# Optimization experiments

Hardware: AMD Instinct MI355X
Metric: run time of the kernel (lower is better)

Reference implementation:

```python
import jax, jax.numpy as jnp
import numpy as np

T, B, H = 512, 128, 512

def setup_inputs() -> dict:
    key = jax.random.key(0)
    k1, k2, k3, k4 = jax.random.split(key, 4)
    s = 1.0 / np.sqrt(H)
    x = jax.random.normal(k1, (T, B, H), dtype=jnp.float32)
    resets = jax.random.randint(k2, (T, B), 0, 2).astype(bool)
    Wi = jax.random.normal(k3, (H, 3 * H), dtype=jnp.float32) * s
    bi = jnp.zeros((3 * H,), dtype=jnp.float32)
    Wh = jax.random.normal(k4, (H, 3 * H), dtype=jnp.float32) * s
    bhn = jnp.zeros((H,), dtype=jnp.float32)
    h0 = jnp.zeros((B, H), dtype=jnp.float32)
    return {"x": x, "resets": resets, "Wi": Wi, "bi": bi, "Wh": Wh, "bhn": bhn, "h0": h0}

def reference(x, resets, Wi, bi, Wh, bhn, h0):
    # Scanned flax GRUCell with per-step carry reset (reset -> zeros carry).
    def step(h, inp):
        xt, rt = inp                                   # xt: [B,H], rt: [B]
        h = jnp.where(rt[:, None], jnp.zeros_like(h), h)
        gi = xt @ Wi + bi                              # [B,3H]
        gh = h @ Wh                                    # [B,3H]
        ir, iz, inn = jnp.split(gi, 3, axis=-1)
        hr, hz, hn = jnp.split(gh, 3, axis=-1)
        r = jax.nn.sigmoid(ir + hr)
        z = jax.nn.sigmoid(iz + hz)
        n = jnp.tanh(inn + r * (hn + bhn))             # bias only on h 'n' gate (flax GRUCell)
        new_h = (1.0 - z) * n + z * h
        return new_h, new_h
    _, ys = jax.lax.scan(step, h0, (x, resets))
    return ys                                          # [T,B,H]
```

## Files before the change

### kernel.cpp

```cpp
#include <hip/hip_runtime.h>


typedef _Float16 f16;
typedef _Float16 f16x8 __attribute__((ext_vector_type(8)));
typedef float f32x4 __attribute__((ext_vector_type(4)));
typedef float f32x16 __attribute__((ext_vector_type(16)));

#define TT 512
#define BB 128
#define HH 512
#define H3 1536
#define TBR 65536
#define NC 64
#define CL 8
#define NR 8192
static const size_t PL = (size_t)TBR * HH;

__device__ __forceinline__ float sigf(float x) { return 1.f / (1.f + __expf(-x)); }

__global__ __launch_bounds__(256) void k_prep(
    const float* __restrict__ Wi, const float* __restrict__ Wh,
    const int* __restrict__ resets,
    f16* __restrict__ WiT, f16* __restrict__ WhT,
    int* __restrict__ fr, int* __restrict__ cnt) {
  int idx = blockIdx.x * 256 + threadIdx.x;
  if (idx < HH * H3) {
    int n = idx >> 9;
    int k = idx & (HH - 1);
    WiT[idx] = (f16)Wi[(size_t)k * H3 + n];
    WhT[idx] = (f16)Wh[(size_t)k * H3 + n];
  }
  if (idx < NR) {
    int c = idx >> 7, b = idx & 127;
    int f = CL;
    for (int s = CL - 1; s >= 0; --s)
      if (resets[(c * CL + s) * BB + b]) f = s;
    fr[idx] = f;
    atomicAdd(&cnt[f], 1);
  }
}

__global__ __launch_bounds__(256) void k_prepB(
    const f16* __restrict__ WhT, f16* __restrict__ WhTf) {
  int u = blockIdx.x * 256 + threadIdx.x;
  int l = u & 63;
  int kb = (u >> 6) & 31;
  int t = u >> 11;
  f16x8 v = *(const f16x8*)(WhT + (size_t)(t * 32 + (l & 31)) * HH +
                            kb * 16 + (l >> 5) * 8);
  *(f16x8*)(WhTf + (size_t)u * 8) = v;
}

__global__ void k_sort(int* __restrict__ cnt) {
  int st = 0;
  cnt[16 + 8] = 0;
  for (int f = 7; f >= 0; --f) {
    st += cnt[f + 1];
    cnt[16 + f] = st;
  }
  for (int f = 1; f <= 8; ++f) cnt[32 + f] = cnt[16 + f];
}

__global__ __launch_bounds__(256) void k_scatter(
    const int* __restrict__ fr, int* __restrict__ cnt, int* __restrict__ list,
    int* __restrict__ slist) {
  int idx = blockIdx.x * 256 + threadIdx.x;
  if (idx < NR) {
    int f = fr[idx];
    if (f >= 1) {
      int pos = atomicAdd(&cnt[32 + f], 1);
      list[pos] = idx;
    }
    int c = idx >> 7;
    if (f == CL && c < NC - 1 && (c == 0 || fr[idx - BB] < CL)) {
      int p = atomicAdd(&cnt[48], 1);
      slist[p] = idx;
    }
  }
}

__global__ __launch_bounds__(256) void k_gemm_gi(
    const float* __restrict__ x, const f16* __restrict__ WiT,
    const float* __restrict__ bi, f16* __restrict__ gi) {
  __shared__ __align__(16) f16 xs[64 * 512];
  const int tid = threadIdx.x;
  const int lane = tid & 63;
  const int w = tid >> 6;
  const size_t i0 = (size_t)blockIdx.x * 64;

  {
    const int row = tid >> 2;
    const int mi = row >> 5;
    const int lin = (row & 31) + ((tid & 1) << 5);
    const int koct = (tid & 3) * 8;
#pragma unroll 4
    for (int kb32 = 0; kb32 < 16; ++kb32) {
      const int k = kb32 * 32 + koct;
      const float* xp = x + (i0 + row) * HH + k;
      float4 v0 = *(const float4*)xp;
      float4 v1 = *(const float4*)(xp + 4);
      f16x8 a8;
      a8[0] = (f16)v0.x; a8[1] = (f16)v0.y; a8[2] = (f16)v0.z; a8[3] = (f16)v0.w;
      a8[4] = (f16)v1.x; a8[5] = (f16)v1.y; a8[6] = (f16)v1.z; a8[7] = (f16)v1.w;
      *(f16x8*)&xs[((k >> 4) * 2 + mi) * 512 + lin * 8] = a8;
    }
  }
  __syncthreads();

  const int ln31 = lane & 31;
  const int kh8 = (lane >> 5) * 8;
  const int r4 = (lane >> 5) * 4;

  for (int jt = 0; jt < 6; ++jt) {
    const int j0 = jt * 256 + w * 64;
    f32x16 acc[2][2] = {};
    const f16* bp0 = WiT + (size_t)(j0 + ln31) * HH + kh8;
    const f16* bp1 = bp0 + (size_t)32 * HH;
#pragma unroll 4
    for (int kb = 0; kb < 32; ++kb) {
      f16x8 af0 = *(const f16x8*)&xs[(kb * 2 + 0) * 512 + lane * 8];
      f16x8 af1 = *(const f16x8*)&xs[(kb * 2 + 1) * 512 + lane * 8];
      f16x8 bf0 = *(const f16x8*)(bp0 + kb * 16);
      f16x8 bf1 = *(const f16x8*)(bp1 + kb * 16);
      acc[0][0] = __builtin_amdgcn_mfma_f32_32x32x16_f16(af0, bf0, acc[0][0], 0, 0, 0);
      acc[0][1] = __builtin_amdgcn_mfma_f32_32x32x16_f16(af0, bf1, acc[0][1], 0, 0, 0);
      acc[1][0] = __builtin_amdgcn_mfma_f32_32x32x16_f16(af1, bf0, acc[1][0], 0, 0, 0);
      acc[1][1] = __builtin_amdgcn_mfma_f32_32x32x16_f16(af1, bf1, acc[1][1], 0, 0, 0);
    }
#pragma unroll
    for (int ni = 0; ni < 2; ++ni) {
      const int j = j0 + ni * 32 + ln31;
      const float bj = bi[j];
      const int p = j >> 9, jj = j & 511;
#pragma unroll
      for (int mi = 0; mi < 2; ++mi)
#pragma unroll
        for (int r = 0; r < 16; ++r) {
          const int row = mi * 32 + (r & 3) + 8 * (r >> 2) + r4;
          gi[(size_t)p * PL + (i0 + row) * HH + jj] =
              (f16)(acc[mi][ni][r] + bj);
        }
    }
  }
}

__global__ __launch_bounds__(256) void k_step0(
    const int* __restrict__ resets, const f16* __restrict__ gi,
    const float* __restrict__ bhn, float* __restrict__ out,
    f16* __restrict__ hA) {
  int gid = blockIdx.x * 256 + threadIdx.x;
  int row = gid >> 6;
  int c8 = (gid & 63) * 8;
  int c = row >> 7, b = row & 127;
  size_t girow = (size_t)c * 1024 + b;
  const f16x8 g0 = *(const f16x8*)(gi + girow * HH + c8);
  const f16x8 g1 = *(const f16x8*)(gi + PL + girow * HH + c8);
  const f16x8 g2 = *(const f16x8*)(gi + 2 * PL + girow * HH + c8);
  const int z1 = resets[(c * CL + 1) * BB + b];
  float4 o[2];
  f16x8 hn;
#pragma unroll
  for (int u = 0; u < 8; ++u) {
    float r = sigf((float)g0[u]);
    float z = sigf((float)g1[u]);
    float n = tanhf((float)g2[u] + r * bhn[c8 + u]);
    float h = (1.f - z) * n;
    ((float*)o)[u] = h;
    hn[u] = z1 ? (f16)0.f : (f16)h;
  }
  *(float4*)(out + girow * HH + c8) = o[0];
  *(float4*)(out + girow * HH + c8 + 4) = o[1];
  *(f16x8*)(hA + (size_t)row * HH + c8) = hn;
}

__global__ __launch_bounds__(256, 2) void k_phase1(
    int s, const int* __restrict__ resets, const f16* __restrict__ WhT,
    const f16* __restrict__ gi, const float* __restrict__ bhn,
    float* __restrict__ out, const f16* __restrict__ hrd,
    f16* __restrict__ hwr) {
  __shared__ __align__(16) f16 As[128 * 40];
  __shared__ __align__(16) f16 Bs[192 * 40];
  const int tid = threadIdx.x;
  const int lane = tid & 63;
  const int w = tid >> 6;
  const int c = blockIdx.x;
  const int j0 = blockIdx.y * 64;
  const int t = c * CL + s;
  const int wm = (w & 1) * 64;
  const int wn = (w >> 1) * 32;
  const int fr = lane & 15;
  const int q8 = (lane >> 4) * 8;

  f32x4 acc[3][4][2] = {};

  for (int kb = 0; kb < 16; ++kb) {
    const int k0 = kb * 32;
#pragma unroll
    for (int uu = 0; uu < 2; ++uu) {
      int u = tid + uu * 256;
      int row = u >> 2, oc = (u & 3) * 8;
      *(f16x8*)&As[row * 40 + oc] =
          *(const f16x8*)(hrd + ((size_t)(c * BB + row)) * HH + k0 + oc);
    }
#pragma unroll
    for (int uu = 0; uu < 3; ++uu) {
      int u = tid + uu * 256;
      int row = u >> 2, oc = (u & 3) * 8;
      int g = row >> 6, j = j0 + (row & 63);
      *(f16x8*)&Bs[row * 40 + oc] =
          *(const f16x8*)(WhT + ((size_t)(g * HH + j)) * HH + k0 + oc);
    }
    __syncthreads();
    f16x8 af[4];
#pragma unroll
    for (int mi = 0; mi < 4; ++mi)
      af[mi] = *(const f16x8*)&As[(wm + mi * 16 + fr) * 40 + q8];
    f16x8 bf[3][2];
#pragma unroll
    for (int g = 0; g < 3; ++g)
#pragma unroll
      for (int ni = 0; ni < 2; ++ni)
        bf[g][ni] = *(const f16x8*)&Bs[(g * 64 + wn + ni * 16 + fr) * 40 + q8];
#pragma unroll
    for (int g = 0; g < 3; ++g)
#pragma unroll
      for (int mi = 0; mi < 4; ++mi)
#pragma unroll
        for (int ni = 0; ni < 2; ++ni)
          acc[g][mi][ni] = __builtin_amdgcn_mfma_f32_16x16x32_f16(
              af[mi], bf[g][ni], acc[g][mi][ni], 0, 0, 0);
    __syncthreads();
  }

  const int trow = (lane >> 4) * 4;
#pragma unroll
  for (int mi = 0; mi < 4; ++mi)
#pragma unroll
    for (int ni = 0; ni < 2; ++ni) {
      const int j = j0 + wn + ni * 16 + fr;
      const float bh = bhn[j];
#pragma unroll
      for (int r = 0; r < 4; ++r) {
        const int b = wm + mi * 16 + trow + r;
        const size_t girow = (size_t)c * 1024 + (size_t)s * BB + b;
        const float gr = (float)gi[girow * HH + j];
        const float gz = (float)gi[PL + girow * HH + j];
        const float gn = (float)gi[2 * PL + girow * HH + j];
        const float hp = (float)hrd[((size_t)(c * BB + b)) * HH + j];
        const float rr = sigf(gr + acc[0][mi][ni][r]);
        const float zz = sigf(gz + acc[1][mi][ni][r]);
        const float nn = tanhf(gn + rr * (acc[2][mi][ni][r] + bh));
        const float hnew = (1.f - zz) * nn + zz * hp;
        out[girow * HH + j] = hnew;
        int zr = (s < 7) ? resets[(t + 1) * BB + b] : 0;
        hwr[((size_t)(c * BB + b)) * HH + j] = zr ? (f16)0.f : (f16)hnew;
      }
    }
}

__global__ __launch_bounds__(256) void k_bound(
    const int* __restrict__ fr, const f16* __restrict__ hend,
    const float* __restrict__ h0, f16* __restrict__ hin) {
  int gid = blockIdx.x * 256 + threadIdx.x;
  int row = gid >> 6;
  int o8 = (gid & 63) * 8;
  int c = row >> 7, b = row & 127;
  if (c == 0) {
    const float* hp = h0 + (size_t)b * HH + o8;
    float4 v0 = *(const float4*)hp;
    float4 v1 = *(const float4*)(hp + 4);
    f16x8 h;
    h[0] = (f16)v0.x; h[1] = (f16)v0.y; h[2] = (f16)v0.z; h[3] = (f16)v0.w;
    h[4] = (f16)v1.x; h[5] = (f16)v1.y; h[6] = (f16)v1.z; h[7] = (f16)v1.w;
    *(f16x8*)(hin + (size_t)row * HH + o8) = h;
  } else if (fr[row - BB] < CL) {
    *(f16x8*)(hin + (size_t)row * HH + o8) =
        *(const f16x8*)(hend + (size_t)(row - BB) * HH + o8);
  }
}

__global__ __launch_bounds__(1024) void k_chain2(
    const int* __restrict__ fr, const f16* __restrict__ hend,
    const f16* __restrict__ WhTf, const f16* __restrict__ gi,
    const float* __restrict__ bhn, const float* __restrict__ h0,
    f16* __restrict__ hin, const int* __restrict__ slist,
    const int* __restrict__ cnt) {
  const int count = cnt[48];
  const int nbat = (count + 31) >> 5;
  __shared__ __align__(16) f16 hsA[32 * 512];
  __shared__ int ch[32];
  __shared__ int anyact;
  const int tid = threadIdx.x;
  const int lane = tid & 63;
  const int w = tid >> 6;
  const int nc = lane & 31;
  const int hi = lane >> 5;

  for (int bat = blockIdx.x; bat < nbat; bat += gridDim.x) {
    if (tid < 32) {
      int r = bat * 32 + tid;
      ch[tid] = (r < count) ? slist[r] : -1;
    }
    __syncthreads();
    for (int u = tid; u < 32 * 64; u += 1024) {
      int m = u >> 6, o8 = (u & 63) * 8;
      int cr = ch[m];
      f16x8 h = {};
      if (cr >= 0) {
        if ((cr >> 7) == 0) {
          const float* hp = h0 + (size_t)(cr & 127) * HH + o8;
          float4 v0 = *(const float4*)hp;
          float4 v1 = *(const float4*)(hp + 4);
          h[0] = (f16)v0.x; h[1] = (f16)v0.y; h[2] = (f16)v0.z; h[3] = (f16)v0.w;
          h[4] = (f16)v1.x; h[5] = (f16)v1.y; h[6] = (f16)v1.z; h[7] = (f16)v1.w;
        } else {
          h = *(const f16x8*)(hend + (size_t)(cr - BB) * HH + o8);
        }
      }
      *(f16x8*)&hsA[(o8 >> 4) * 512 + (m + ((o8 >> 3) & 1) * 32) * 8] = h;
    }
    __syncthreads();

    while (true) {
      for (int s = 0; s < CL; ++s) {
        f32x16 a0 = {}, a1 = {}, a2 = {};
        const f16* b0p = WhTf + ((size_t)(w)*32 * 64 + lane) * 8;
        const f16* b1p = WhTf + ((size_t)(16 + w) * 32 * 64 + lane) * 8;
        const f16* b2p = WhTf + ((size_t)(32 + w) * 32 * 64 + lane) * 8;
#pragma unroll 4
        for (int kb = 0; kb < 32; ++kb) {
          f16x8 af = *(const f16x8*)&hsA[kb * 512 + lane * 8];
          f16x8 bf0 = *(const f16x8*)(b0p + (size_t)kb * 512);
          f16x8 bf1 = *(const f16x8*)(b1p + (size_t)kb * 512);
          f16x8 bf2 = *(const f16x8*)(b2p + (size_t)kb * 512);
          a0 = __builtin_amdgcn_mfma_f32_32x32x16_f16(af, bf0, a0, 0, 0, 0);
          a1 = __builtin_amdgcn_mfma_f32_32x32x16_f16(af, bf1, a1, 0, 0, 0);
          a2 = __builtin_amdgcn_mfma_f32_32x32x16_f16(af, bf2, a2, 0, 0, 0);
        }
        __syncthreads();
        const int j = w * 32 + nc;
        const float bh = bhn[j];
#pragma unroll
        for (int r = 0; r < 16; ++r) {
          const int m = (r & 3) + 8 * (r >> 2) + 4 * hi;
          const int cr = ch[m];
          const size_t girow =
              (cr >= 0)
                  ? ((size_t)(cr >> 7) * 1024 + (size_t)s * BB + (cr & 127))
                  : 0;
          const float gr = (float)gi[girow * HH + j];
          const float gz = (float)gi[PL + girow * HH + j];
          const float gn = (float)gi[2 * PL + girow * HH + j];
          const int ha =
              (j >> 4) * 512 + (m + ((j >> 3) & 1) * 32) * 8 + (j & 7);
          const float hp = (float)hsA[ha];
          const float rr = sigf(gr + a0[r]);
          const float zz = sigf(gz + a1[r]);
          const float nn = tanhf(gn + rr * (a2[r] + bh));
          hsA[ha] = (f16)((1.f - zz) * nn + zz * hp);
        }
        __syncthreads();
      }
      for (int u = tid; u < 32 * 64; u += 1024) {
        int m = u >> 6, o8 = (u & 63) * 8;
        int cr = ch[m];
        if (cr >= 0) {
          f16x8 h = *(const f16x8*)&hsA[(o8 >> 4) * 512 +
                                        (m + ((o8 >> 3) & 1) * 32) * 8];
          *(f16x8*)(hin + (size_t)(cr + BB) * HH + o8) = h;
        }
      }
      if (tid == 0) anyact = 0;
      __syncthreads();
      if (tid < 32) {
        int cr = ch[tid];
        if (cr >= 0) {
          int nrow = cr + BB;
          if (fr[nrow] == CL && (nrow >> 7) < NC - 1) {
            ch[tid] = nrow;
            atomicAdd(&anyact, 1);
          } else {
            ch[tid] = -1;
          }
        }
      }
      __syncthreads();
      if (anyact == 0) break;
    }
    __syncthreads();
  }
}

__global__ __launch_bounds__(256) void k_phase3(
    int s, const int* __restrict__ cnt, const int* __restrict__ list,
    const f16* __restrict__ WhT, const f16* __restrict__ gi,
    const float* __restrict__ bhn, float* __restrict__ out,
    f16* __restrict__ hph) {
  const int count = cnt[16 + s];
  const int r0 = blockIdx.x * 16;
  if (r0 >= count) return;
  __shared__ __align__(16) f16 As[16 * 520];
  __shared__ int rows[16];
  const int tid = threadIdx.x;
  const int lane = tid & 63;
  const int w = tid >> 6;
  if (tid < 16) rows[tid] = (r0 + tid < count) ? list[r0 + tid] : -1;
  __syncthreads();
#pragma unroll
  for (int uu = 0; uu < 4; ++uu) {
    int u = tid + uu * 256;
    int row = u >> 6, oc = (u & 63) * 8;
    int rid = rows[row];
    f16x8 v = {};
    if (rid >= 0) v = *(const f16x8*)(hph + (size_t)rid * HH + oc);
    *(f16x8*)&As[row * 520 + oc] = v;
  }
  __syncthreads();
  const int fr16 = lane & 15;
  const int q8 = (lane >> 4) * 8;
  const int trow = (lane >> 4) * 4;
  for (int jt = 0; jt < 8; ++jt) {
    const int jb = w * 128 + jt * 16;
    f32x4 a0 = {}, a1 = {}, a2 = {};
#pragma unroll 4
    for (int kb = 0; kb < 16; ++kb) {
      const int k0 = kb * 32;
      f16x8 af = *(const f16x8*)&As[fr16 * 520 + k0 + q8];
      f16x8 b0 = *(const f16x8*)(WhT + ((size_t)(jb + fr16)) * HH + k0 + q8);
      f16x8 b1 = *(const f16x8*)(WhT + ((size_t)(HH + jb + fr16)) * HH + k0 + q8);
      f16x8 b2 = *(const f16x8*)(WhT + ((size_t)(2 * HH + jb + fr16)) * HH + k0 + q8);
      a0 = __builtin_amdgcn_mfma_f32_16x16x32_f16(af, b0, a0, 0, 0, 0);
      a1 = __builtin_amdgcn_mfma_f32_16x16x32_f16(af, b1, a1, 0, 0, 0);
      a2 = __builtin_amdgcn_mfma_f32_16x16x32_f16(af, b2, a2, 0, 0, 0);
    }
    const int j = jb + fr16;
    const float bh = bhn[j];
#pragma unroll
    for (int r = 0; r < 4; ++r) {
      const int rid = rows[trow + r];
      if (rid < 0) continue;
      const int c = rid >> 7, b = rid & 127;
      const size_t girow = (size_t)(c * CL + s) * BB + b;
      const float gr = (float)gi[girow * HH + j];
      const float gz = (float)gi[PL + girow * HH + j];
      const float gn = (float)gi[2 * PL + girow * HH + j];
      const float hp = (float)hph[(size_t)rid * HH + j];
      const float rr = sigf(gr + a0[r]);
      const float zz = sigf(gz + a1[r]);
      const float nn = tanhf(gn + rr * (a2[r] + bh));
      const float hnew = (1.f - zz) * nn + zz * hp;
      out[girow * HH + j] = hnew;
      hph[(size_t)rid * HH + j] = (f16)hnew;
    }
  }
}

extern "C" void kernel_launch(void* const* d_in, const int* in_sizes, int n_in,
                              void* d_out, int out_size, void* d_ws, size_t ws_size,
                              hipStream_t stream) {
  const float* x = (const float*)d_in[0];
  const int* resets = (const int*)d_in[1];
  const float* Wi = (const float*)d_in[2];
  const float* bi = (const float*)d_in[3];
  const float* Wh = (const float*)d_in[4];
  const float* bhn = (const float*)d_in[5];
  const float* h0 = (const float*)d_in[6];
  float* out = (float*)d_out;

  char* ws = (char*)d_ws;
  size_t off = 0;
  f16* gi = (f16*)(ws + off);    off += 3 * PL * sizeof(f16);
  f16* WiT = (f16*)(ws + off);   off += (size_t)HH * H3 * sizeof(f16);
  f16* WhT = (f16*)(ws + off);   off += (size_t)HH * H3 * sizeof(f16);
  f16* WhTf = (f16*)(ws + off);  off += (size_t)HH * H3 * sizeof(f16);
  f16* hA = (f16*)(ws + off);    off += (size_t)NR * HH * sizeof(f16);
  f16* hB = (f16*)(ws + off);    off += (size_t)NR * HH * sizeof(f16);
  f16* hin = (f16*)(ws + off);   off += (size_t)NR * HH * sizeof(f16);
  int* fr = (int*)(ws + off);    off += NR * sizeof(int);
  int* list = (int*)(ws + off);  off += NR * sizeof(int);
  int* slist = (int*)(ws + off); off += NR * sizeof(int);
  int* cnt = (int*)(ws + off);   off += 64 * sizeof(int);
  (void)ws_size; (void)in_sizes; (void)n_in; (void)out_size;

  hipMemsetAsync(cnt, 0, 64 * sizeof(int), stream);
  k_prep<<<dim3(3072), 256, 0, stream>>>(Wi, Wh, resets, WiT, WhT, fr, cnt);
  k_prepB<<<dim3(384), 256, 0, stream>>>(WhT, WhTf);
  k_sort<<<dim3(1), 1, 0, stream>>>(cnt);
  k_scatter<<<dim3(32), 256, 0, stream>>>(fr, cnt, list, slist);
  k_gemm_gi<<<dim3(TBR / 64), 256, 0, stream>>>(x, WiT, bi, gi);
  k_step0<<<dim3(NR * 64 / 256), 256, 0, stream>>>(resets, gi, bhn, out, hA);
  for (int s = 1; s < CL; ++s) {
    const f16* hrd = (s & 1) ? hA : hB;
    f16* hwr = (s & 1) ? hB : hA;
    k_phase1<<<dim3(NC, 8), 256, 0, stream>>>(s, resets, WhT, gi, bhn, out, hrd, hwr);
  }
  k_bound<<<dim3(NR * 64 / 256), 256, 0, stream>>>(fr, hB, h0, hin);
  k_chain2<<<dim3(4), 1024, 0, stream>>>(fr, hB, WhTf, gi, bhn, h0, hin, slist, cnt);
  for (int s = 0; s < CL; ++s)
    k_phase3<<<dim3(NR / 16), 256, 0, stream>>>(s, cnt, list, WhT, gi, bhn, out, hin);
}
```

Baseline: 1.813 ms.

## Use fragment-packed weights in gi GEMM and phase1, swizzle chain LDS layout

Adds a fragment-packed copy of Wi (WiTf) so the input-projection GEMM reads contiguous per-lane weight fragments instead of strided rows. Rewrites k_phase1 as a 1024-thread block that handles 32 rows and all 512 columns, using the packed Wh fragments and 32x32 MFMAs instead of tiling through LDS with 16x16 MFMAs. Applies an XOR swizzle to the hidden-state LDS layout in k_chain2 to reduce bank conflicts. The cost is extra prep work and workspace for the packed Wi, and phase1 now launches 256 large blocks, each re-reading the full Wh from cache.

```diff
diff --git a/kernel.cpp b/kernel.cpp
--- a/kernel.cpp
+++ b/kernel.cpp
@@ -41,14 +41,19 @@
 }
 
 __global__ __launch_bounds__(256) void k_prepB(
-    const f16* __restrict__ WhT, f16* __restrict__ WhTf) {
-  int u = blockIdx.x * 256 + threadIdx.x;
+    const f16* __restrict__ WhT, const f16* __restrict__ WiT,
+    f16* __restrict__ WhTf, f16* __restrict__ WiTf) {
+  int idx = blockIdx.x * 256 + threadIdx.x;
+  const f16* src = WhT;
+  f16* dst = WhTf;
+  int u = idx;
+  if (idx >= 98304) { src = WiT; dst = WiTf; u = idx - 98304; }
   int l = u & 63;
   int kb = (u >> 6) & 31;
   int t = u >> 11;
-  f16x8 v = *(const f16x8*)(WhT + (size_t)(t * 32 + (l & 31)) * HH +
+  f16x8 v = *(const f16x8*)(src + (size_t)(t * 32 + (l & 31)) * HH +
                             kb * 16 + (l >> 5) * 8);
-  *(f16x8*)(WhTf + (size_t)u * 8) = v;
+  *(f16x8*)(dst + (size_t)u * 8) = v;
 }
 
 __global__ void k_sort(int* __restrict__ cnt) {
@@ -80,7 +85,7 @@
 }
 
 __global__ __launch_bounds__(256) void k_gemm_gi(
-    const float* __restrict__ x, const f16* __restrict__ WiT,
+    const float* __restrict__ x, const f16* __restrict__ WiTf,
     const float* __restrict__ bi, f16* __restrict__ gi) {
   __shared__ __align__(16) f16 xs[64 * 512];
   const int tid = threadIdx.x;
@@ -108,20 +113,19 @@
   __syncthreads();
 
   const int ln31 = lane & 31;
-  const int kh8 = (lane >> 5) * 8;
   const int r4 = (lane >> 5) * 4;
 
   for (int jt = 0; jt < 6; ++jt) {
-    const int j0 = jt * 256 + w * 64;
+    const int t0 = jt * 8 + w * 2;
     f32x16 acc[2][2] = {};
-    const f16* bp0 = WiT + (size_t)(j0 + ln31) * HH + kh8;
-    const f16* bp1 = bp0 + (size_t)32 * HH;
+    const f16* bp0 = WiTf + ((size_t)t0 * 2048 + lane) * 8;
+    const f16* bp1 = WiTf + ((size_t)(t0 + 1) * 2048 + lane) * 8;
 #pragma unroll 4
     for (int kb = 0; kb < 32; ++kb) {
       f16x8 af0 = *(const f16x8*)&xs[(kb * 2 + 0) * 512 + lane * 8];
       f16x8 af1 = *(const f16x8*)&xs[(kb * 2 + 1) * 512 + lane * 8];
-      f16x8 bf0 = *(const f16x8*)(bp0 + kb * 16);
-      f16x8 bf1 = *(const f16x8*)(bp1 + kb * 16);
+      f16x8 bf0 = *(const f16x8*)(bp0 + (size_t)kb * 512);
+      f16x8 bf1 = *(const f16x8*)(bp1 + (size_t)kb * 512);
       acc[0][0] = __builtin_amdgcn_mfma_f32_32x32x16_f16(af0, bf0, acc[0][0], 0, 0, 0);
       acc[0][1] = __builtin_amdgcn_mfma_f32_32x32x16_f16(af0, bf1, acc[0][1], 0, 0, 0);
       acc[1][0] = __builtin_amdgcn_mfma_f32_32x32x16_f16(af1, bf0, acc[1][0], 0, 0, 0);
@@ -129,7 +133,7 @@
     }
 #pragma unroll
     for (int ni = 0; ni < 2; ++ni) {
-      const int j = j0 + ni * 32 + ln31;
+      const int j = (t0 + ni) * 32 + ln31;
       const float bj = bi[j];
       const int p = j >> 9, jj = j & 511;
 #pragma unroll
@@ -173,89 +177,63 @@
   *(f16x8*)(hA + (size_t)row * HH + c8) = hn;
 }
 
-__global__ __launch_bounds__(256, 2) void k_phase1(
-    int s, const int* __restrict__ resets, const f16* __restrict__ WhT,
+__global__ __launch_bounds__(1024) void k_phase1(
+    int s, const int* __restrict__ resets, const f16* __restrict__ WhTf,
     const f16* __restrict__ gi, const float* __restrict__ bhn,
     float* __restrict__ out, const f16* __restrict__ hrd,
     f16* __restrict__ hwr) {
-  __shared__ __align__(16) f16 As[128 * 40];
-  __shared__ __align__(16) f16 Bs[192 * 40];
+  __shared__ __align__(16) f16 hsA[32 * 512];
   const int tid = threadIdx.x;
   const int lane = tid & 63;
   const int w = tid >> 6;
-  const int c = blockIdx.x;
-  const int j0 = blockIdx.y * 64;
+  const int gr0 = blockIdx.x * 32;
+  const int c = gr0 >> 7;
   const int t = c * CL + s;
-  const int wm = (w & 1) * 64;
-  const int wn = (w >> 1) * 32;
-  const int fr = lane & 15;
-  const int q8 = (lane >> 4) * 8;
-
-  f32x4 acc[3][4][2] = {};
-
-  for (int kb = 0; kb < 16; ++kb) {
-    const int k0 = kb * 32;
-#pragma unroll
-    for (int uu = 0; uu < 2; ++uu) {
-      int u = tid + uu * 256;
-      int row = u >> 2, oc = (u & 3) * 8;
-      *(f16x8*)&As[row * 40 + oc] =
-          *(const f16x8*)(hrd + ((size_t)(c * BB + row)) * HH + k0 + oc);
-    }
-#pragma unroll
-    for (int uu = 0; uu < 3; ++uu) {
-      int u = tid + uu * 256;
-      int row = u >> 2, oc = (u & 3) * 8;
-      int g = row >> 6, j = j0 + (row & 63);
-      *(f16x8*)&Bs[row * 40 + oc] =
-          *(const f16x8*)(WhT + ((size_t)(g * HH + j)) * HH + k0 + oc);
-    }
-    __syncthreads();
-    f16x8 af[4];
-#pragma unroll
-    for (int mi = 0; mi < 4; ++mi)
-      af[mi] = *(const f16x8*)&As[(wm + mi * 16 + fr) * 40 + q8];
-    f16x8 bf[3][2];
-#pragma unroll
-    for (int g = 0; g < 3; ++g)
-#pragma unroll
-      for (int ni = 0; ni < 2; ++ni)
-        bf[g][ni] = *(const f16x8*)&Bs[(g * 64 + wn + ni * 16 + fr) * 40 + q8];
-#pragma unroll
-    for (int g = 0; g < 3; ++g)
-#pragma unroll
-      for (int mi = 0; mi < 4; ++mi)
-#pragma unroll
-        for (int ni = 0; ni < 2; ++ni)
-          acc[g][mi][ni] = __builtin_amdgcn_mfma_f32_16x16x32_f16(
-              af[mi], bf[g][ni], acc[g][mi][ni], 0, 0, 0);
-    __syncthreads();
-  }
-
-  const int trow = (lane >> 4) * 4;
-#pragma unroll
-  for (int mi = 0; mi < 4; ++mi)
-#pragma unroll
-    for (int ni = 0; ni < 2; ++ni) {
-      const int j = j0 + wn + ni * 16 + fr;
-      const float bh = bhn[j];
-#pragma unroll
-      for (int r = 0; r < 4; ++r) {
-        const int b = wm + mi * 16 + trow + r;
-        const size_t girow = (size_t)c * 1024 + (size_t)s * BB + b;
-        const float gr = (float)gi[girow * HH + j];
-        const float gz = (float)gi[PL + girow * HH + j];
-        const float gn = (float)gi[2 * PL + girow * HH + j];
-        const float hp = (float)hrd[((size_t)(c * BB + b)) * HH + j];
-        const float rr = sigf(gr + acc[0][mi][ni][r]);
-        const float zz = sigf(gz + acc[1][mi][ni][r]);
-        const float nn = tanhf(gn + rr * (acc[2][mi][ni][r] + bh));
-        const float hnew = (1.f - zz) * nn + zz * hp;
-        out[girow * HH + j] = hnew;
-        int zr = (s < 7) ? resets[(t + 1) * BB + b] : 0;
-        hwr[((size_t)(c * BB + b)) * HH + j] = zr ? (f16)0.f : (f16)hnew;
-      }
-    }
+
+  for (int u = tid; u < 32 * 64; u += 1024) {
+    int m = u >> 6, o8 = (u & 63) * 8;
+    f16x8 h = *(const f16x8*)(hrd + (size_t)(gr0 + m) * HH + o8);
+    *(f16x8*)&hsA[(o8 >> 4) * 512 + (m + ((o8 >> 3) & 1) * 32) * 8] = h;
+  }
+  __syncthreads();
+
+  f32x16 a0 = {}, a1 = {}, a2 = {};
+  const f16* b0p = WhTf + ((size_t)w * 2048 + lane) * 8;
+  const f16* b1p = WhTf + ((size_t)(16 + w) * 2048 + lane) * 8;
+  const f16* b2p = WhTf + ((size_t)(32 + w) * 2048 + lane) * 8;
+#pragma unroll 4
+  for (int kb = 0; kb < 32; ++kb) {
+    f16x8 af = *(const f16x8*)&hsA[kb * 512 + lane * 8];
+    f16x8 bf0 = *(const f16x8*)(b0p + (size_t)kb * 512);
+    f16x8 bf1 = *(const f16x8*)(b1p + (size_t)kb * 512);
+    f16x8 bf2 = *(const f16x8*)(b2p + (size_t)kb * 512);
+    a0 = __builtin_amdgcn_mfma_f32_32x32x16_f16(af, bf0, a0, 0, 0, 0);
+    a1 = __builtin_amdgcn_mfma_f32_32x32x16_f16(af, bf1, a1, 0, 0, 0);
+    a2 = __builtin_amdgcn_mfma_f32_32x32x16_f16(af, bf2, a2, 0, 0, 0);
+  }
+
+  const int nc = lane & 31;
+  const int hi = lane >> 5;
+  const int j = w * 32 + nc;
+  const float bh = bhn[j];
+#pragma unroll
+  for (int r = 0; r < 16; ++r) {
+    const int m = (r & 3) + 8 * (r >> 2) + 4 * hi;
+    const int gr = gr0 + m;
+    const int b = gr & 127;
+    const size_t girow = (size_t)c * 1024 + (size_t)s * BB + b;
+    const float grv = (float)gi[girow * HH + j];
+    const float gzv = (float)gi[PL + girow * HH + j];
+    const float gnv = (float)gi[2 * PL + girow * HH + j];
+    const float hp = (float)hrd[(size_t)gr * HH + j];
+    const float rr = sigf(grv + a0[r]);
+    const float zz = sigf(gzv + a1[r]);
+    const float nn = tanhf(gnv + rr * (a2[r] + bh));
+    const float hnew = (1.f - zz) * nn + zz * hp;
+    out[girow * HH + j] = hnew;
+    int zr = (s < 7) ? resets[(t + 1) * BB + b] : 0;
+    hwr[(size_t)gr * HH + j] = zr ? (f16)0.f : (f16)hnew;
+  }
 }
 
 __global__ __launch_bounds__(256) void k_bound(
@@ -295,6 +273,8 @@
   const int w = tid >> 6;
   const int nc = lane & 31;
   const int hi = lane >> 5;
+  const int sl0 = (lane ^ (lane >> 5)) * 8;
+  const int sl1 = sl0 ^ 16;
 
   for (int bat = blockIdx.x; bat < nbat; bat += gridDim.x) {
     if (tid < 32) {
@@ -303,33 +283,35 @@
     }
     __syncthreads();
     for (int u = tid; u < 32 * 64; u += 1024) {
-      int m = u >> 6, o8 = (u & 63) * 8;
+      int m = u >> 6, oct = u & 63;
       int cr = ch[m];
       f16x8 h = {};
       if (cr >= 0) {
         if ((cr >> 7) == 0) {
-          const float* hp = h0 + (size_t)(cr & 127) * HH + o8;
+          const float* hp = h0 + (size_t)(cr & 127) * HH + oct * 8;
           float4 v0 = *(const float4*)hp;
           float4 v1 = *(const float4*)(hp + 4);
           h[0] = (f16)v0.x; h[1] = (f16)v0.y; h[2] = (f16)v0.z; h[3] = (f16)v0.w;
           h[4] = (f16)v1.x; h[5] = (f16)v1.y; h[6] = (f16)v1.z; h[7] = (f16)v1.w;
         } else {
-          h = *(const f16x8*)(hend + (size_t)(cr - BB) * HH + o8);
+          h = *(const f16x8*)(hend + (size_t)(cr - BB) * HH + oct * 8);
         }
       }
-      *(f16x8*)&hsA[(o8 >> 4) * 512 + (m + ((o8 >> 3) & 1) * 32) * 8] = h;
+      int slot = (m + (oct & 1) * 32) ^ (oct & 1) ^ (((oct >> 1) & 1) << 1);
+      *(f16x8*)&hsA[(oct >> 1) * 512 + slot * 8] = h;
     }
     __syncthreads();
 
     while (true) {
       for (int s = 0; s < CL; ++s) {
         f32x16 a0 = {}, a1 = {}, a2 = {};
-        const f16* b0p = WhTf + ((size_t)(w)*32 * 64 + lane) * 8;
-        const f16* b1p = WhTf + ((size_t)(16 + w) * 32 * 64 + lane) * 8;
-        const f16* b2p = WhTf + ((size_t)(32 + w) * 32 * 64 + lane) * 8;
+        const f16* b0p = WhTf + ((size_t)w * 2048 + lane) * 8;
+        const f16* b1p = WhTf + ((size_t)(16 + w) * 2048 + lane) * 8;
+        const f16* b2p = WhTf + ((size_t)(32 + w) * 2048 + lane) * 8;
 #pragma unroll 4
         for (int kb = 0; kb < 32; ++kb) {
-          f16x8 af = *(const f16x8*)&hsA[kb * 512 + lane * 8];
+          const int sb = (kb & 1) ? sl1 : sl0;
+          f16x8 af = *(const f16x8*)&hsA[kb * 512 + sb];
           f16x8 bf0 = *(const f16x8*)(b0p + (size_t)kb * 512);
           f16x8 bf1 = *(const f16x8*)(b1p + (size_t)kb * 512);
           f16x8 bf2 = *(const f16x8*)(b2p + (size_t)kb * 512);
@@ -340,6 +322,9 @@
         __syncthreads();
         const int j = w * 32 + nc;
         const float bh = bhn[j];
+        const int jhi = (j >> 3) & 1;
+        const int jkb = j >> 4;
+        const int swz = jhi ^ ((jkb & 1) << 1);
 #pragma unroll
         for (int r = 0; r < 16; ++r) {
           const int m = (r & 3) + 8 * (r >> 2) + 4 * hi;
@@ -348,26 +333,26 @@
               (cr >= 0)
                   ? ((size_t)(cr >> 7) * 1024 + (size_t)s * BB + (cr & 127))
                   : 0;
-          const float gr = (float)gi[girow * HH + j];
-          const float gz = (float)gi[PL + girow * HH + j];
-          const float gn = (float)gi[2 * PL + girow * HH + j];
-          const int ha =
-              (j >> 4) * 512 + (m + ((j >> 3) & 1) * 32) * 8 + (j & 7);
+          const float grv = (float)gi[girow * HH + j];
+          const float gzv = (float)gi[PL + girow * HH + j];
+          const float gnv = (float)gi[2 * PL + girow * HH + j];
+          const int slot = (m + jhi * 32) ^ swz;
+          const int ha = jkb * 512 + slot * 8 + (j & 7);
           const float hp = (float)hsA[ha];
-          const float rr = sigf(gr + a0[r]);
-          const float zz = sigf(gz + a1[r]);
-          const float nn = tanhf(gn + rr * (a2[r] + bh));
+          const float rr = sigf(grv + a0[r]);
+          const float zz = sigf(gzv + a1[r]);
+          const float nn = tanhf(gnv + rr * (a2[r] + bh));
           hsA[ha] = (f16)((1.f - zz) * nn + zz * hp);
         }
         __syncthreads();
       }
       for (int u = tid; u < 32 * 64; u += 1024) {
-        int m = u >> 6, o8 = (u & 63) * 8;
+        int m = u >> 6, oct = u & 63;
         int cr = ch[m];
         if (cr >= 0) {
-          f16x8 h = *(const f16x8*)&hsA[(o8 >> 4) * 512 +
-                                        (m + ((o8 >> 3) & 1) * 32) * 8];
-          *(f16x8*)(hin + (size_t)(cr + BB) * HH + o8) = h;
+          int slot = (m + (oct & 1) * 32) ^ (oct & 1) ^ (((oct >> 1) & 1) << 1);
+          f16x8 h = *(const f16x8*)&hsA[(oct >> 1) * 512 + slot * 8];
+          *(f16x8*)(hin + (size_t)(cr + BB) * HH + oct * 8) = h;
         }
       }
       if (tid == 0) anyact = 0;
@@ -473,6 +458,7 @@
   f16* WiT = (f16*)(ws + off);   off += (size_t)HH * H3 * sizeof(f16);
   f16* WhT = (f16*)(ws + off);   off += (size_t)HH * H3 * sizeof(f16);
   f16* WhTf = (f16*)(ws + off);  off += (size_t)HH * H3 * sizeof(f16);
+  f16* WiTf = (f16*)(ws + off);  off += (size_t)HH * H3 * sizeof(f16);
   f16* hA = (f16*)(ws + off);    off += (size_t)NR * HH * sizeof(f16);
   f16* hB = (f16*)(ws + off);    off += (size_t)NR * HH * sizeof(f16);
   f16* hin = (f16*)(ws + off);   off += (size_t)NR * HH * sizeof(f16);
@@ -484,15 +470,16 @@
 
   hipMemsetAsync(cnt, 0, 64 * sizeof(int), stream);
   k_prep<<<dim3(3072), 256, 0, stream>>>(Wi, Wh, resets, WiT, WhT, fr, cnt);
-  k_prepB<<<dim3(384), 256, 0, stream>>>(WhT, WhTf);
+  k_prepB<<<dim3(768), 256, 0, stream>>>(WhT, WiT, WhTf, WiTf);
   k_sort<<<dim3(1), 1, 0, stream>>>(cnt);
   k_scatter<<<dim3(32), 256, 0, stream>>>(fr, cnt, list, slist);
-  k_gemm_gi<<<dim3(TBR / 64), 256, 0, stream>>>(x, WiT, bi, gi);
+  k_gemm_gi<<<dim3(TBR / 64), 256, 0, stream>>>(x, WiTf, bi, gi);
   k_step0<<<dim3(NR * 64 / 256), 256, 0, stream>>>(resets, gi, bhn, out, hA);
   for (int s = 1; s < CL; ++s) {
     const f16* hrd = (s & 1) ? hA : hB;
     f16* hwr = (s & 1) ? hB : hA;
-    k_phase1<<<dim3(NC, 8), 256, 0, stream>>>(s, resets, WhT, gi, bhn, out, hrd, hwr);
+    k_phase1<<<dim3(NR / 32), 1024, 0, stream>>>(s, resets, WhTf, gi, bhn, out,
+                                                 hrd, hwr);
   }
   k_bound<<<dim3(NR * 64 / 256), 256, 0, stream>>>(fr, hB, h0, hin);
   k_chain2<<<dim3(4), 1024, 0, stream>>>(fr, hB, WhTf, gi, bhn, h0, hin, slist, cnt);
```

After: 1.723 ms. 5.0% less time.
